# Kernel tuning notes

Hardware: AMD Instinct MI355X
Metric: run time of the kernel (lower is better)

Reference implementation:

```python
import jax, jax.numpy as jnp
import numpy as np

TTT_LR = 0.01
LN_EPS = 1e-5


def setup_inputs() -> dict:
    key = jax.random.key(0)
    ks = jax.random.split(key, 4)
    B, S, D, DS = 4, 2048, 1024, 64
    sc = 1.0 / np.sqrt(D).astype(np.float32)
    return {
        "x": jax.random.normal(ks[0], (B, S, D), dtype=jnp.float32),
        "Wk": jax.random.normal(ks[1], (DS, D), dtype=jnp.float32) * sc,
        "bk": jnp.zeros((DS,), jnp.float32),
        "Wv": jax.random.normal(ks[2], (D, D), dtype=jnp.float32) * sc,
        "bv": jnp.zeros((D,), jnp.float32),
        "Wq": jax.random.normal(ks[3], (DS, D), dtype=jnp.float32) * sc,
        "bq": jnp.zeros((DS,), jnp.float32),
        "gamma": jnp.ones((D,), jnp.float32),
        "beta": jnp.zeros((D,), jnp.float32),
    }


def reference(x, Wk, bk, Wv, bv, Wq, bq, gamma, beta):
    B, S, D = x.shape
    DS = Wk.shape[0]
    # LayerNorm over last dim
    mu = jnp.mean(x, axis=-1, keepdims=True)
    var = jnp.mean((x - mu) ** 2, axis=-1, keepdims=True)
    h = (x - mu) * jax.lax.rsqrt(var + LN_EPS) * gamma + beta
    # projections: keys/queries (B,S,DS), values (B,S,D)
    keys = jnp.einsum('bsd,ed->bse', h, Wk) + bk
    values = jnp.einsum('bsd,ed->bse', h, Wv) + bv
    queries = jnp.einsum('bsd,ed->bse', h, Wq) + bq

    def step(W, qkv):
        # W: (B, D, DS) fast-weight state
        q_t, k_t, v_t = qkv  # (B,DS), (B,DS), (B,D)
        y_t = jnp.einsum('bds,bs->bd', W, q_t)      # read with query
        pred = jnp.einsum('bds,bs->bd', W, k_t)     # predict with key
        err = pred - v_t                             # (B, D)
        W = W - TTT_LR * err[:, :, None] * k_t[:, None, :]  # rank-1 grad step
        return W, y_t

    W0 = jnp.zeros((B, D, DS), x.dtype)
    # scan over time: inputs as (S, B, ...)
    qs = jnp.swapaxes(queries, 0, 1)
    ks_ = jnp.swapaxes(keys, 0, 1)
    vs = jnp.swapaxes(values, 0, 1)
    _, ys = jax.lax.scan(step, W0, (qs, ks_, vs))   # ys: (S, B, D)
    y = jnp.swapaxes(ys, 0, 1)
    return x + y
```

## Files before the change

### kernel.cpp

```cpp
#include <hip/hip_runtime.h>
#include <hip/hip_bf16.h>

#define TTT_LR 0.01f
#define LN_EPS 1e-5f

#define BB 4
#define SS 2048
#define DD 1024
#define DSZ 64
#define CHUNK 64
#define NC (SS / CHUNK)
#define NCAT 1152
#define MiB (1024ull * 1024ull)

typedef __hip_bfloat16 bf16;
typedef __bf16 bf16x8 __attribute__((ext_vector_type(8)));
typedef float f32x4 __attribute__((ext_vector_type(4)));

__device__ __forceinline__ void gload_lds16(const void* g, void* l) {
    __builtin_amdgcn_global_load_lds(
        (const __attribute__((address_space(1))) unsigned int*)g,
        (__attribute__((address_space(3))) unsigned int*)l, 16, 0, 0);
}

__global__ __launch_bounds__(256) void cvt_cat_kernel(
    const float* __restrict__ Wk, const float* __restrict__ Wq,
    const float* __restrict__ Wv, bf16* __restrict__ Wcat)
{
    const int i = blockIdx.x * 256 + threadIdx.x;
    if (i >= NCAT * DD / 4) return;
    const int idx = i * 4;
    const int row = idx >> 10, col = idx & 1023;
    const float* src = (row < 64)  ? (Wk + (size_t)row * DD)
                     : (row < 128) ? (Wq + (size_t)(row - 64) * DD)
                                   : (Wv + (size_t)(row - 128) * DD);
    float4 v = *reinterpret_cast<const float4*>(src + col);
    bf16 h4[4] = {__float2bfloat16(v.x), __float2bfloat16(v.y),
                  __float2bfloat16(v.z), __float2bfloat16(v.w)};
    *reinterpret_cast<ushort4*>(Wcat + idx) = *reinterpret_cast<ushort4*>(h4);
}

__global__ __launch_bounds__(256) void ln_kernel(
    const float* __restrict__ x, const float* __restrict__ gamma,
    const float* __restrict__ beta, bf16* __restrict__ hb)
{
    __shared__ float wsum[4], wsum2[4];
    const int row = blockIdx.x, tid = threadIdx.x;
    const int lane = tid & 63, wave = tid >> 6;

    float4 v0 = *reinterpret_cast<const float4*>(x + (size_t)row * DD + tid * 4);
    float s = v0.x + v0.y + v0.z + v0.w;
    float s2 = fmaf(v0.x, v0.x, fmaf(v0.y, v0.y, fmaf(v0.z, v0.z, v0.w * v0.w)));
    #pragma unroll
    for (int off = 32; off > 0; off >>= 1) {
        s  += __shfl_down(s, off, 64);
        s2 += __shfl_down(s2, off, 64);
    }
    if (lane == 0) { wsum[wave] = s; wsum2[wave] = s2; }
    __syncthreads();
    s  = wsum[0] + wsum[1] + wsum[2] + wsum[3];
    s2 = wsum2[0] + wsum2[1] + wsum2[2] + wsum2[3];
    const float mu = s * (1.0f / DD);
    const float rs = rsqrtf(s2 * (1.0f / DD) - mu * mu + LN_EPS);

    float4 g  = *reinterpret_cast<const float4*>(gamma + tid * 4);
    float4 be = *reinterpret_cast<const float4*>(beta + tid * 4);
    bf16 h4[4];
    h4[0] = __float2bfloat16((v0.x - mu) * rs * g.x + be.x);
    h4[1] = __float2bfloat16((v0.y - mu) * rs * g.y + be.y);
    h4[2] = __float2bfloat16((v0.z - mu) * rs * g.z + be.z);
    h4[3] = __float2bfloat16((v0.w - mu) * rs * g.w + be.w);
    *reinterpret_cast<ushort4*>(hb + (size_t)row * DD + tid * 4) =
        *reinterpret_cast<ushort4*>(h4);
}

__global__ __launch_bounds__(256) void kqv_kernel(
    const bf16* __restrict__ h, const bf16* __restrict__ Wcat,
    const float* __restrict__ bk, const float* __restrict__ bq,
    const float* __restrict__ bv,
    float* __restrict__ kbuf, float* __restrict__ qbuf, bf16* __restrict__ vbuf16)
{
    __shared__ bf16 Ash[128 * 64];
    __shared__ bf16 Bsh[128 * 64];
    const int tid = threadIdx.x, lane = tid & 63, wave = tid >> 6;
    const int m = lane & 15, quad = lane >> 4;
    const int wr = wave >> 1, wc = wave & 1;
    const int m0 = blockIdx.y * 128;
    const int n0 = blockIdx.x * 128;

    const int srow = wave * 8 + (lane >> 3);
    const int scb = lane & 7;

    f32x4 acc[4][4] = {};

    for (int k0 = 0; k0 < DD; k0 += 64) {
        __syncthreads();
        #pragma unroll
        for (int i = 0; i < 4; ++i) {
            const int row = i * 32 + srow;
            const int g16 = scb ^ (row & 7);
            gload_lds16(h    + (size_t)(m0 + row) * DD + k0 + g16 * 8,
                        (char*)Ash + (size_t)(i * 32 + wave * 8) * 128);
            gload_lds16(Wcat + (size_t)(n0 + row) * DD + k0 + g16 * 8,
                        (char*)Bsh + (size_t)(i * 32 + wave * 8) * 128);
        }
        __syncthreads();
        #pragma unroll
        for (int ks = 0; ks < 2; ++ks) {
            bf16x8 af[4], bfr[4];
            #pragma unroll
            for (int mt = 0; mt < 4; ++mt) {
                const int row = wr * 64 + mt * 16 + m;
                const int kb = (ks * 4 + quad) ^ (row & 7);
                af[mt] = *reinterpret_cast<const bf16x8*>(&Ash[row * 64 + kb * 8]);
            }
            #pragma unroll
            for (int nt = 0; nt < 4; ++nt) {
                const int row = wc * 64 + nt * 16 + m;
                const int kb = (ks * 4 + quad) ^ (row & 7);
                bfr[nt] = *reinterpret_cast<const bf16x8*>(&Bsh[row * 64 + kb * 8]);
            }
            #pragma unroll
            for (int mt = 0; mt < 4; ++mt)
                #pragma unroll
                for (int nt = 0; nt < 4; ++nt)
                    acc[mt][nt] = __builtin_amdgcn_mfma_f32_16x16x32_bf16(
                        af[mt], bfr[nt], acc[mt][nt], 0, 0, 0);
        }
    }

    #pragma unroll
    for (int nt = 0; nt < 4; ++nt) {
        const int n = n0 + wc * 64 + nt * 16 + m;
        if (n < 64) {
            const float bias = bk[n];
            #pragma unroll
            for (int mt = 0; mt < 4; ++mt) {
                const int row = m0 + wr * 64 + mt * 16 + quad * 4;
                #pragma unroll
                for (int r = 0; r < 4; ++r)
                    kbuf[(size_t)(row + r) * DSZ + n] = acc[mt][nt][r] + bias;
            }
        } else if (n < 128) {
            const float bias = bq[n - 64];
            #pragma unroll
            for (int mt = 0; mt < 4; ++mt) {
                const int row = m0 + wr * 64 + mt * 16 + quad * 4;
                #pragma unroll
                for (int r = 0; r < 4; ++r)
                    qbuf[(size_t)(row + r) * DSZ + (n - 64)] = acc[mt][nt][r] + bias;
            }
        } else {
            const float bias = bv[n - 128];
            #pragma unroll
            for (int mt = 0; mt < 4; ++mt) {
                const int row = m0 + wr * 64 + mt * 16 + quad * 4;
                #pragma unroll
                for (int r = 0; r < 4; ++r)
                    vbuf16[(size_t)(row + r) * DD + (n - 128)] =
                        __float2bfloat16(acc[mt][nt][r] + bias);
            }
        }
    }
}

__global__ __launch_bounds__(256) void prep_kernel(
    const float* __restrict__ kbuf, const float* __restrict__ qbuf,
    bf16* __restrict__ Mb16, bf16* __restrict__ AMb16,
    bf16* __restrict__ Bb16, bf16* __restrict__ Qtb16, bf16* __restrict__ Ktb16)
{
    __shared__ bf16 K16[64 * 72];
    __shared__ bf16 Kt16[64 * 72];
    __shared__ bf16 Q16[64 * 72];
    __shared__ bf16 Astl[64 * 72];
    __shared__ bf16 Minv16[64 * 72];
    __shared__ bf16 MinvT16[64 * 72];
    __shared__ bf16 BnegT[64 * 72];
    __shared__ float Gf[64 * 65];
    __shared__ float Mf[64 * 65];

    const int c = blockIdx.x, b = blockIdx.y;
    const int tid = threadIdx.x, lane = tid & 63, w = tid >> 6;
    const int m = lane & 15, quad = lane >> 4;
    const float* kp = kbuf + ((size_t)b * SS + c * 64) * DSZ;
    const float* qp = qbuf + ((size_t)b * SS + c * 64) * DSZ;
    const size_t cb = ((size_t)b * NC + c) * 4096;

    #pragma unroll
    for (int it = 0; it < 4; ++it) {
        const int f4 = tid + it * 256;
        const int t = f4 >> 4;
        const int s = (f4 & 15) * 4;
        float4 kv = *reinterpret_cast<const float4*>(kp + t * DSZ + s);
        float4 qv = *reinterpret_cast<const float4*>(qp + t * DSZ + s);
        bf16 kb4[4] = {__float2bfloat16(kv.x), __float2bfloat16(kv.y),
                       __float2bfloat16(kv.z), __float2bfloat16(kv.w)};
        bf16 qb4[4] = {__float2bfloat16(qv.x), __float2bfloat16(qv.y),
                       __float2bfloat16(qv.z), __float2bfloat16(qv.w)};
        *reinterpret_cast<ushort4*>(&K16[t * 72 + s]) = *reinterpret_cast<ushort4*>(kb4);
        *reinterpret_cast<ushort4*>(&Q16[t * 72 + s]) = *reinterpret_cast<ushort4*>(qb4);
        #pragma unroll
        for (int i = 0; i < 4; ++i) Kt16[(s + i) * 72 + t] = kb4[i];
    }
    __syncthreads();

    bf16x8 afK[2], afQ[2], bfK[4][2];
    #pragma unroll
    for (int ks = 0; ks < 2; ++ks) {
        afK[ks] = *reinterpret_cast<const bf16x8*>(&K16[(w * 16 + m) * 72 + ks * 32 + quad * 8]);
        afQ[ks] = *reinterpret_cast<const bf16x8*>(&Q16[(w * 16 + m) * 72 + ks * 32 + quad * 8]);
        #pragma unroll
        for (int nt = 0; nt < 4; ++nt)
            bfK[nt][ks] = *reinterpret_cast<const bf16x8*>(&K16[(nt * 16 + m) * 72 + ks * 32 + quad * 8]);
    }
    f32x4 gacc[4] = {}, aacc[4] = {};
    #pragma unroll
    for (int ks = 0; ks < 2; ++ks)
        #pragma unroll
        for (int nt = 0; nt < 4; ++nt) {
            gacc[nt] = __builtin_amdgcn_mfma_f32_16x16x32_bf16(afK[ks], bfK[nt][ks], gacc[nt], 0, 0, 0);
            aacc[nt] = __builtin_amdgcn_mfma_f32_16x16x32_bf16(afQ[ks], bfK[nt][ks], aacc[nt], 0, 0, 0);
        }
    #pragma unroll
    for (int nt = 0; nt < 4; ++nt)
        #pragma unroll
        for (int r = 0; r < 4; ++r) {
            const int t = w * 16 + quad * 4 + r, j = nt * 16 + m;
            Gf[t * 65 + j] = TTT_LR * gacc[nt][r];
            Astl[t * 72 + j] = __float2bfloat16(j < t ? aacc[nt][r] : 0.f);
        }
    __syncthreads();

    if (tid < 64) {
        for (int t = 0; t < 64; ++t) {
            float acc = (t == tid) ? 1.f : 0.f;
            for (int i = 0; i < t; ++i)
                acc = fmaf(-Gf[t * 65 + i], Mf[i * 65 + tid], acc);
            Mf[t * 65 + tid] = acc;
        }
    }
    __syncthreads();

    #pragma unroll
    for (int it = 0; it < 16; ++it) {
        const int e = tid + it * 256;
        const int t = e >> 6, j = e & 63;
        const bf16 vb = __float2bfloat16(TTT_LR * Mf[t * 65 + j]);
        Minv16[t * 72 + j] = vb;
        MinvT16[j * 72 + t] = vb;
        Mb16[cb + e] = vb;
        const unsigned short ku =
            *reinterpret_cast<const unsigned short*>(&Kt16[t * 72 + j]) ^ 0x8000u;
        *reinterpret_cast<unsigned short*>(&Ktb16[cb + e]) = ku;
    }
    __syncthreads();

    bf16x8 afM[2], afA[2], bfKt[4][2], bfMt[4][2];
    #pragma unroll
    for (int ks = 0; ks < 2; ++ks) {
        afM[ks] = *reinterpret_cast<const bf16x8*>(&Minv16[(w * 16 + m) * 72 + ks * 32 + quad * 8]);
        afA[ks] = *reinterpret_cast<const bf16x8*>(&Astl[(w * 16 + m) * 72 + ks * 32 + quad * 8]);
        #pragma unroll
        for (int nt = 0; nt < 4; ++nt) {
            bfKt[nt][ks] = *reinterpret_cast<const bf16x8*>(&Kt16[(nt * 16 + m) * 72 + ks * 32 + quad * 8]);
            bfMt[nt][ks] = *reinterpret_cast<const bf16x8*>(&MinvT16[(nt * 16 + m) * 72 + ks * 32 + quad * 8]);
        }
    }
    f32x4 bacc[4] = {};
    #pragma unroll
    for (int ks = 0; ks < 2; ++ks)
        #pragma unroll
        for (int nt = 0; nt < 4; ++nt)
            bacc[nt] = __builtin_amdgcn_mfma_f32_16x16x32_bf16(afM[ks], bfKt[nt][ks], bacc[nt], 0, 0, 0);
    #pragma unroll
    for (int nt = 0; nt < 4; ++nt)
        #pragma unroll
        for (int r = 0; r < 4; ++r) {
            const int t = w * 16 + quad * 4 + r, s = nt * 16 + m;
            Bb16[cb + t * 64 + s] = __float2bfloat16(bacc[nt][r]);
            BnegT[s * 72 + t] = __float2bfloat16(-bacc[nt][r]);
        }
    __syncthreads();

    f32x4 qtacc[4], amacc[4] = {};
    #pragma unroll
    for (int nt = 0; nt < 4; ++nt)
        #pragma unroll
        for (int r = 0; r < 4; ++r)
            qtacc[nt][r] = qp[(w * 16 + quad * 4 + r) * DSZ + nt * 16 + m];
    #pragma unroll
    for (int ks = 0; ks < 2; ++ks)
        #pragma unroll
        for (int nt = 0; nt < 4; ++nt) {
            const bf16x8 bfBn = *reinterpret_cast<const bf16x8*>(
                &BnegT[(nt * 16 + m) * 72 + ks * 32 + quad * 8]);
            qtacc[nt] = __builtin_amdgcn_mfma_f32_16x16x32_bf16(afA[ks], bfBn, qtacc[nt], 0, 0, 0);
            amacc[nt] = __builtin_amdgcn_mfma_f32_16x16x32_bf16(afA[ks], bfMt[nt][ks], amacc[nt], 0, 0, 0);
        }
    #pragma unroll
    for (int nt = 0; nt < 4; ++nt)
        #pragma unroll
        for (int r = 0; r < 4; ++r) {
            const int t = w * 16 + quad * 4 + r, s = nt * 16 + m;
            Qtb16[cb + t * 64 + s] = __float2bfloat16(qtacc[nt][r]);
            AMb16[cb + t * 64 + s] = __float2bfloat16(amacc[nt][r]);
        }
}

__global__ __launch_bounds__(256) void usolve_kernel(
    const bf16* __restrict__ Mb16, const bf16* __restrict__ AMb16,
    const bf16* __restrict__ v16, const float* __restrict__ x,
    bf16* __restrict__ U16, float* __restrict__ out)
{
    __shared__ bf16 Vsh[64 * 136];
    const int tid = threadIdx.x, lane = tid & 63, w = tid >> 6;
    const int m = lane & 15, quad = lane >> 4;
    const int dblk = blockIdx.x, c = blockIdx.y, b = blockIdx.z;
    const int d0 = dblk * 128;
    const size_t cb = ((size_t)b * NC + c) * 4096;
    const size_t rowbase = (size_t)b * SS + (size_t)c * 64;

    #pragma unroll
    for (int it = 0; it < 4; ++it) {
        const int j = (tid >> 4) + it * 16;
        const int dd = (tid & 15) * 8;
        bf16x8 vv = *reinterpret_cast<const bf16x8*>(
            v16 + (rowbase + j) * DD + d0 + dd);
        *reinterpret_cast<bf16x8*>(&Vsh[j * 136 + dd]) = vv;
    }

    bf16x8 fM[4][2], fA[4][2];
    #pragma unroll
    for (int mt = 0; mt < 4; ++mt)
        #pragma unroll
        for (int ks = 0; ks < 2; ++ks) {
            const int off = (mt * 16 + m) * 64 + ks * 32 + quad * 8;
            fM[mt][ks] = *reinterpret_cast<const bf16x8*>(Mb16 + cb + off);
            fA[mt][ks] = *reinterpret_cast<const bf16x8*>(AMb16 + cb + off);
        }
    __syncthreads();

    f32x4 uacc[4][2] = {}, yacc[4][2] = {};
    #pragma unroll
    for (int ks = 0; ks < 2; ++ks)
        #pragma unroll
        for (int nt = 0; nt < 2; ++nt) {
            const int d = w * 32 + nt * 16 + m;
            alignas(16) unsigned short tmp[8];
            #pragma unroll
            for (int jj = 0; jj < 8; ++jj)
                tmp[jj] = *reinterpret_cast<const unsigned short*>(
                    &Vsh[(ks * 32 + quad * 8 + jj) * 136 + d]);
            bf16x8 bfrag = *reinterpret_cast<bf16x8*>(tmp);
            #pragma unroll
            for (int mt = 0; mt < 4; ++mt) {
                uacc[mt][nt] = __builtin_amdgcn_mfma_f32_16x16x32_bf16(
                    fM[mt][ks], bfrag, uacc[mt][nt], 0, 0, 0);
                yacc[mt][nt] = __builtin_amdgcn_mfma_f32_16x16x32_bf16(
                    fA[mt][ks], bfrag, yacc[mt][nt], 0, 0, 0);
            }
        }

    #pragma unroll
    for (int mt = 0; mt < 4; ++mt)
        #pragma unroll
        for (int nt = 0; nt < 2; ++nt) {
            const int dcol = d0 + w * 32 + nt * 16 + m;
            #pragma unroll
            for (int r = 0; r < 4; ++r) {
                const int t = mt * 16 + quad * 4 + r;
                const size_t off = (rowbase + t) * DD + dcol;
                U16[off] = __float2bfloat16(uacc[mt][nt][r]);
                out[off] = x[off] + yacc[mt][nt][r];
            }
        }
}

__global__ __launch_bounds__(256) void seq_kernel(
    const bf16* __restrict__ Bb16, const bf16* __restrict__ Qtb16,
    const bf16* __restrict__ Ktb16, const bf16* __restrict__ U16,
    float* __restrict__ out)
{
    __shared__ bf16 Zsh[16][72];
    __shared__ bf16 Psh[16][72];
    const int dblk = blockIdx.x, b = blockIdx.y;
    const int tid = threadIdx.x, lane = tid & 63, w = tid >> 6;
    const int m = lane & 15, quad = lane >> 4;
    const int d0 = dblk * 16;
    const int arow = w * 16 + m;
    const int trow = w * 16 + quad * 4;

    f32x4 zacc = {0.f, 0.f, 0.f, 0.f};
    for (int i = tid; i < 16 * 72; i += 256)
        (&Zsh[0][0])[i] = __float2bfloat16(0.f);

    for (int c = 0; c < NC; ++c) {
        const size_t cb = ((size_t)b * NC + c) * 4096;
        const size_t gbase = ((size_t)b * SS + (size_t)c * 64 + trow) * DD + d0 + m;
        const bf16x8 aB0 = *reinterpret_cast<const bf16x8*>(Bb16 + cb + arow * 64 + quad * 8);
        const bf16x8 aB1 = *reinterpret_cast<const bf16x8*>(Bb16 + cb + arow * 64 + 32 + quad * 8);
        const bf16x8 aQ0 = *reinterpret_cast<const bf16x8*>(Qtb16 + cb + arow * 64 + quad * 8);
        const bf16x8 aQ1 = *reinterpret_cast<const bf16x8*>(Qtb16 + cb + arow * 64 + 32 + quad * 8);
        const bf16x8 aK0 = *reinterpret_cast<const bf16x8*>(Ktb16 + cb + arow * 64 + quad * 8);
        const bf16x8 aK1 = *reinterpret_cast<const bf16x8*>(Ktb16 + cb + arow * 64 + 32 + quad * 8);
        float uld[4], old[4];
        #pragma unroll
        for (int r = 0; r < 4; ++r) {
            uld[r] = __bfloat162float(U16[gbase + (size_t)r * DD]);
            old[r] = out[gbase + (size_t)r * DD];
        }

        __syncthreads();
        const bf16x8 z0 = *reinterpret_cast<const bf16x8*>(&Zsh[m][quad * 8]);
        const bf16x8 z1 = *reinterpret_cast<const bf16x8*>(&Zsh[m][32 + quad * 8]);
        f32x4 pacc = {0.f, 0.f, 0.f, 0.f};
        f32x4 yacc = {0.f, 0.f, 0.f, 0.f};
        pacc = __builtin_amdgcn_mfma_f32_16x16x32_bf16(aB0, z0, pacc, 0, 0, 0);
        pacc = __builtin_amdgcn_mfma_f32_16x16x32_bf16(aB1, z1, pacc, 0, 0, 0);
        yacc = __builtin_amdgcn_mfma_f32_16x16x32_bf16(aQ0, z0, yacc, 0, 0, 0);
        yacc = __builtin_amdgcn_mfma_f32_16x16x32_bf16(aQ1, z1, yacc, 0, 0, 0);

        alignas(8) bf16 pb[4];
        #pragma unroll
        for (int r = 0; r < 4; ++r) {
            out[gbase + (size_t)r * DD] = old[r] + yacc[r];
            pb[r] = __float2bfloat16(pacc[r] - uld[r]);
        }
        *reinterpret_cast<uint2*>(&Psh[m][trow]) = *reinterpret_cast<uint2*>(pb);

        __syncthreads();
        const bf16x8 p0 = *reinterpret_cast<const bf16x8*>(&Psh[m][quad * 8]);
        const bf16x8 p1 = *reinterpret_cast<const bf16x8*>(&Psh[m][32 + quad * 8]);
        zacc = __builtin_amdgcn_mfma_f32_16x16x32_bf16(aK0, p0, zacc, 0, 0, 0);
        zacc = __builtin_amdgcn_mfma_f32_16x16x32_bf16(aK1, p1, zacc, 0, 0, 0);

        alignas(8) bf16 zb[4];
        #pragma unroll
        for (int r = 0; r < 4; ++r) zb[r] = __float2bfloat16(zacc[r]);
        *reinterpret_cast<uint2*>(&Zsh[m][trow]) = *reinterpret_cast<uint2*>(zb);
    }
}

extern "C" void kernel_launch(void* const* d_in, const int* in_sizes, int n_in,
                              void* d_out, int out_size, void* d_ws, size_t ws_size,
                              hipStream_t stream)
{
    const float* x     = (const float*)d_in[0];
    const float* Wk    = (const float*)d_in[1];
    const float* bk    = (const float*)d_in[2];
    const float* Wv    = (const float*)d_in[3];
    const float* bv    = (const float*)d_in[4];
    const float* Wq    = (const float*)d_in[5];
    const float* bq    = (const float*)d_in[6];
    const float* gamma = (const float*)d_in[7];
    const float* beta  = (const float*)d_in[8];

    char* ws = (char*)d_ws;
    const size_t WCAT_B = (size_t)NCAT * DD * 2;
    bf16*  hb    = (bf16*)ws;
    bf16*  Bb16  = (bf16*)(ws + 0 * MiB);
    bf16*  Qtb16 = (bf16*)(ws + 1 * MiB);
    bf16*  Ktb16 = (bf16*)(ws + 2 * MiB);
    bf16*  Mb16  = (bf16*)(ws + 3 * MiB);
    bf16*  AMb16 = (bf16*)(ws + 4 * MiB);
    bf16*  Wcat  = (bf16*)(ws + 16 * MiB);
    float* kbuf  = (float*)(ws + 16 * MiB + WCAT_B);
    float* qbuf  = (float*)(ws + 18 * MiB + WCAT_B);
    bf16*  v16   = (bf16*)(ws + 20 * MiB + WCAT_B);
    bf16*  U16   = (bf16*)(ws + 36 * MiB + WCAT_B);

    cvt_cat_kernel<<<(NCAT * DD / 4 + 255) / 256, 256, 0, stream>>>(Wk, Wq, Wv, Wcat);
    ln_kernel<<<BB * SS, 256, 0, stream>>>(x, gamma, beta, hb);
    kqv_kernel<<<dim3(NCAT / 128, BB * SS / 128), 256, 0, stream>>>(
        hb, Wcat, bk, bq, bv, kbuf, qbuf, v16);
    prep_kernel<<<dim3(NC, BB), 256, 0, stream>>>(
        kbuf, qbuf, Mb16, AMb16, Bb16, Qtb16, Ktb16);
    usolve_kernel<<<dim3(DD / 128, NC, BB), 256, 0, stream>>>(
        Mb16, AMb16, v16, x, U16, (float*)d_out);
    seq_kernel<<<dim3(DD / 16, BB), 256, 0, stream>>>(
        Bb16, Qtb16, Ktb16, U16, (float*)d_out);
}
```

Baseline: 235.8 us.

## Fuse intra-chunk U/Y solve into the sequential chunk scan kernel

```diff
diff --git a/kernel.cpp b/kernel.cpp
--- a/kernel.cpp
+++ b/kernel.cpp
@@ -307,82 +307,15 @@
         }
 }
 
-__global__ __launch_bounds__(256) void usolve_kernel(
+__global__ __launch_bounds__(256) void scan2_kernel(
     const bf16* __restrict__ Mb16, const bf16* __restrict__ AMb16,
-    const bf16* __restrict__ v16, const float* __restrict__ x,
-    bf16* __restrict__ U16, float* __restrict__ out)
-{
-    __shared__ bf16 Vsh[64 * 136];
-    const int tid = threadIdx.x, lane = tid & 63, w = tid >> 6;
-    const int m = lane & 15, quad = lane >> 4;
-    const int dblk = blockIdx.x, c = blockIdx.y, b = blockIdx.z;
-    const int d0 = dblk * 128;
-    const size_t cb = ((size_t)b * NC + c) * 4096;
-    const size_t rowbase = (size_t)b * SS + (size_t)c * 64;
-
-    #pragma unroll
-    for (int it = 0; it < 4; ++it) {
-        const int j = (tid >> 4) + it * 16;
-        const int dd = (tid & 15) * 8;
-        bf16x8 vv = *reinterpret_cast<const bf16x8*>(
-            v16 + (rowbase + j) * DD + d0 + dd);
-        *reinterpret_cast<bf16x8*>(&Vsh[j * 136 + dd]) = vv;
-    }
-
-    bf16x8 fM[4][2], fA[4][2];
-    #pragma unroll
-    for (int mt = 0; mt < 4; ++mt)
-        #pragma unroll
-        for (int ks = 0; ks < 2; ++ks) {
-            const int off = (mt * 16 + m) * 64 + ks * 32 + quad * 8;
-            fM[mt][ks] = *reinterpret_cast<const bf16x8*>(Mb16 + cb + off);
-            fA[mt][ks] = *reinterpret_cast<const bf16x8*>(AMb16 + cb + off);
-        }
-    __syncthreads();
-
-    f32x4 uacc[4][2] = {}, yacc[4][2] = {};
-    #pragma unroll
-    for (int ks = 0; ks < 2; ++ks)
-        #pragma unroll
-        for (int nt = 0; nt < 2; ++nt) {
-            const int d = w * 32 + nt * 16 + m;
-            alignas(16) unsigned short tmp[8];
-            #pragma unroll
-            for (int jj = 0; jj < 8; ++jj)
-                tmp[jj] = *reinterpret_cast<const unsigned short*>(
-                    &Vsh[(ks * 32 + quad * 8 + jj) * 136 + d]);
-            bf16x8 bfrag = *reinterpret_cast<bf16x8*>(tmp);
-            #pragma unroll
-            for (int mt = 0; mt < 4; ++mt) {
-                uacc[mt][nt] = __builtin_amdgcn_mfma_f32_16x16x32_bf16(
-                    fM[mt][ks], bfrag, uacc[mt][nt], 0, 0, 0);
-                yacc[mt][nt] = __builtin_amdgcn_mfma_f32_16x16x32_bf16(
-                    fA[mt][ks], bfrag, yacc[mt][nt], 0, 0, 0);
-            }
-        }
-
-    #pragma unroll
-    for (int mt = 0; mt < 4; ++mt)
-        #pragma unroll
-        for (int nt = 0; nt < 2; ++nt) {
-            const int dcol = d0 + w * 32 + nt * 16 + m;
-            #pragma unroll
-            for (int r = 0; r < 4; ++r) {
-                const int t = mt * 16 + quad * 4 + r;
-                const size_t off = (rowbase + t) * DD + dcol;
-                U16[off] = __float2bfloat16(uacc[mt][nt][r]);
-                out[off] = x[off] + yacc[mt][nt][r];
-            }
-        }
-}
-
-__global__ __launch_bounds__(256) void seq_kernel(
     const bf16* __restrict__ Bb16, const bf16* __restrict__ Qtb16,
-    const bf16* __restrict__ Ktb16, const bf16* __restrict__ U16,
-    float* __restrict__ out)
+    const bf16* __restrict__ Ktb16, const bf16* __restrict__ v16,
+    const float* __restrict__ x, float* __restrict__ out)
 {
     __shared__ bf16 Zsh[16][72];
     __shared__ bf16 Psh[16][72];
+    __shared__ bf16 Vsh[2][16][72];
     const int dblk = blockIdx.x, b = blockIdx.y;
     const int tid = threadIdx.x, lane = tid & 63, w = tid >> 6;
     const int m = lane & 15, quad = lane >> 4;
@@ -390,41 +323,62 @@
     const int arow = w * 16 + m;
     const int trow = w * 16 + quad * 4;
 
+    const int vj = tid >> 2;
+    const int vd = (tid & 3) * 4;
+
     f32x4 zacc = {0.f, 0.f, 0.f, 0.f};
     for (int i = tid; i < 16 * 72; i += 256)
         (&Zsh[0][0])[i] = __float2bfloat16(0.f);
 
     for (int c = 0; c < NC; ++c) {
         const size_t cb = ((size_t)b * NC + c) * 4096;
-        const size_t gbase = ((size_t)b * SS + (size_t)c * 64 + trow) * DD + d0 + m;
+        const size_t rowbase = (size_t)b * SS + (size_t)c * 64;
+        const size_t gbase = (rowbase + trow) * DD + d0 + m;
+
+        const bf16x8 aM0 = *reinterpret_cast<const bf16x8*>(Mb16 + cb + arow * 64 + quad * 8);
+        const bf16x8 aM1 = *reinterpret_cast<const bf16x8*>(Mb16 + cb + arow * 64 + 32 + quad * 8);
+        const bf16x8 aA0 = *reinterpret_cast<const bf16x8*>(AMb16 + cb + arow * 64 + quad * 8);
+        const bf16x8 aA1 = *reinterpret_cast<const bf16x8*>(AMb16 + cb + arow * 64 + 32 + quad * 8);
         const bf16x8 aB0 = *reinterpret_cast<const bf16x8*>(Bb16 + cb + arow * 64 + quad * 8);
         const bf16x8 aB1 = *reinterpret_cast<const bf16x8*>(Bb16 + cb + arow * 64 + 32 + quad * 8);
         const bf16x8 aQ0 = *reinterpret_cast<const bf16x8*>(Qtb16 + cb + arow * 64 + quad * 8);
         const bf16x8 aQ1 = *reinterpret_cast<const bf16x8*>(Qtb16 + cb + arow * 64 + 32 + quad * 8);
         const bf16x8 aK0 = *reinterpret_cast<const bf16x8*>(Ktb16 + cb + arow * 64 + quad * 8);
         const bf16x8 aK1 = *reinterpret_cast<const bf16x8*>(Ktb16 + cb + arow * 64 + 32 + quad * 8);
-        float uld[4], old[4];
-        #pragma unroll
-        for (int r = 0; r < 4; ++r) {
-            uld[r] = __bfloat162float(U16[gbase + (size_t)r * DD]);
-            old[r] = out[gbase + (size_t)r * DD];
-        }
+        alignas(8) bf16 va[4];
+        *reinterpret_cast<uint2*>(va) = *reinterpret_cast<const uint2*>(
+            v16 + (rowbase + vj) * DD + d0 + vd);
+        float xld[4];
+        #pragma unroll
+        for (int r = 0; r < 4; ++r) xld[r] = x[gbase + (size_t)r * DD];
+
+        #pragma unroll
+        for (int i = 0; i < 4; ++i) Vsh[c & 1][vd + i][vj] = va[i];
 
         __syncthreads();
         const bf16x8 z0 = *reinterpret_cast<const bf16x8*>(&Zsh[m][quad * 8]);
         const bf16x8 z1 = *reinterpret_cast<const bf16x8*>(&Zsh[m][32 + quad * 8]);
+        const bf16x8 v0 = *reinterpret_cast<const bf16x8*>(&Vsh[c & 1][m][quad * 8]);
+        const bf16x8 v1 = *reinterpret_cast<const bf16x8*>(&Vsh[c & 1][m][32 + quad * 8]);
+
+        f32x4 uacc = {0.f, 0.f, 0.f, 0.f};
+        f32x4 yi   = {0.f, 0.f, 0.f, 0.f};
         f32x4 pacc = {0.f, 0.f, 0.f, 0.f};
-        f32x4 yacc = {0.f, 0.f, 0.f, 0.f};
+        f32x4 yc   = {0.f, 0.f, 0.f, 0.f};
+        uacc = __builtin_amdgcn_mfma_f32_16x16x32_bf16(aM0, v0, uacc, 0, 0, 0);
+        uacc = __builtin_amdgcn_mfma_f32_16x16x32_bf16(aM1, v1, uacc, 0, 0, 0);
+        yi   = __builtin_amdgcn_mfma_f32_16x16x32_bf16(aA0, v0, yi, 0, 0, 0);
+        yi   = __builtin_amdgcn_mfma_f32_16x16x32_bf16(aA1, v1, yi, 0, 0, 0);
         pacc = __builtin_amdgcn_mfma_f32_16x16x32_bf16(aB0, z0, pacc, 0, 0, 0);
         pacc = __builtin_amdgcn_mfma_f32_16x16x32_bf16(aB1, z1, pacc, 0, 0, 0);
-        yacc = __builtin_amdgcn_mfma_f32_16x16x32_bf16(aQ0, z0, yacc, 0, 0, 0);
-        yacc = __builtin_amdgcn_mfma_f32_16x16x32_bf16(aQ1, z1, yacc, 0, 0, 0);
+        yc   = __builtin_amdgcn_mfma_f32_16x16x32_bf16(aQ0, z0, yc, 0, 0, 0);
+        yc   = __builtin_amdgcn_mfma_f32_16x16x32_bf16(aQ1, z1, yc, 0, 0, 0);
 
         alignas(8) bf16 pb[4];
         #pragma unroll
         for (int r = 0; r < 4; ++r) {
-            out[gbase + (size_t)r * DD] = old[r] + yacc[r];
-            pb[r] = __float2bfloat16(pacc[r] - uld[r]);
+            out[gbase + (size_t)r * DD] = xld[r] + yi[r] + yc[r];
+            pb[r] = __float2bfloat16(pacc[r] - uacc[r]);
         }
         *reinterpret_cast<uint2*>(&Psh[m][trow]) = *reinterpret_cast<uint2*>(pb);
 
@@ -467,7 +421,6 @@
     float* kbuf  = (float*)(ws + 16 * MiB + WCAT_B);
     float* qbuf  = (float*)(ws + 18 * MiB + WCAT_B);
     bf16*  v16   = (bf16*)(ws + 20 * MiB + WCAT_B);
-    bf16*  U16   = (bf16*)(ws + 36 * MiB + WCAT_B);
 
     cvt_cat_kernel<<<(NCAT * DD / 4 + 255) / 256, 256, 0, stream>>>(Wk, Wq, Wv, Wcat);
     ln_kernel<<<BB * SS, 256, 0, stream>>>(x, gamma, beta, hb);
@@ -475,8 +428,6 @@
         hb, Wcat, bk, bq, bv, kbuf, qbuf, v16);
     prep_kernel<<<dim3(NC, BB), 256, 0, stream>>>(
         kbuf, qbuf, Mb16, AMb16, Bb16, Qtb16, Ktb16);
-    usolve_kernel<<<dim3(DD / 128, NC, BB), 256, 0, stream>>>(
-        Mb16, AMb16, v16, x, U16, (float*)d_out);
-    seq_kernel<<<dim3(DD / 16, BB), 256, 0, stream>>>(
-        Bb16, Qtb16, Ktb16, U16, (float*)d_out);
-}
+    scan2_kernel<<<dim3(DD / 16, BB), 256, 0, stream>>>(
+        Mb16, AMb16, Bb16, Qtb16, Ktb16, v16, x, (float*)d_out);
+}
```

Result: no change. 233.4 us (-1.0%).
